# Kernel tuning notes

Hardware: AMD Instinct MI355X
Metric: run time of the kernel (lower is better)

Reference implementation:

```python
import jax, jax.numpy as jnp
import numpy as np

N, E, G, H = 4096, 8192, 64, 128  # nodes, edges, graphs, hidden dim
NODE_DIM, EDGE_DIM = 11, 5


def _linear_params(key, fan_in, fan_out):
    kw, kb = jax.random.split(key)
    s = 1.0 / np.sqrt(fan_in)
    w = jax.random.uniform(kw, (fan_in, fan_out), minval=-s, maxval=s, dtype=jnp.float32)
    b = jax.random.uniform(kb, (fan_out,), minval=-s, maxval=s, dtype=jnp.float32)
    return w, b


def setup_inputs() -> dict:
    key = jax.random.key(0)
    ks = jax.random.split(key, 10)
    x = jax.random.normal(ks[0], (N, NODE_DIM), dtype=jnp.float32)
    edge_attr = jax.random.normal(ks[1], (E, EDGE_DIM), dtype=jnp.float32)
    edge_index = jax.random.randint(ks[2], (2, E), 0, N, dtype=jnp.int64)
    batch = jnp.sort(jax.random.randint(ks[3], (N,), 0, G, dtype=jnp.int64))
    # preprocess MLP: node_dim -> 128 -> 128
    p1_w, p1_b = _linear_params(ks[4], NODE_DIM, H)
    p2_w, p2_b = _linear_params(ks[5], H, H)
    # edge net: edge_dim -> 128 -> 256 -> 128 -> 128*128 (ReLU between, none after last)
    e1_w, e1_b = _linear_params(ks[6], EDGE_DIM, 128)
    e2_w, e2_b = _linear_params(ks[7], 128, 256)
    e3_w, e3_b = _linear_params(ks[8], 256, 128)
    e4_w, e4_b = _linear_params(ks[9], 128, H * H)
    return {"x": x, "edge_attr": edge_attr, "edge_index": edge_index, "batch": batch,
            "p1_w": p1_w, "p1_b": p1_b, "p2_w": p2_w, "p2_b": p2_b,
            "e1_w": e1_w, "e1_b": e1_b, "e2_w": e2_w, "e2_b": e2_b,
            "e3_w": e3_w, "e3_b": e3_b, "e4_w": e4_w, "e4_b": e4_b}


def reference(x, edge_attr, edge_index, batch,
              p1_w, p1_b, p2_w, p2_b,
              e1_w, e1_b, e2_w, e2_b, e3_w, e3_b, e4_w, e4_b):
    # node preprocess MLP (maps 11-dim features to 128 so NNConv dims are consistent)
    h = jax.nn.relu(x @ p1_w + p1_b) @ p2_w + p2_b  # [N, H]
    # edge network -> per-edge weight matrix [E, H, H]
    e = jax.nn.relu(edge_attr @ e1_w + e1_b)
    e = jax.nn.relu(e @ e2_w + e2_b)
    e = jax.nn.relu(e @ e3_w + e3_b)
    W = (e @ e4_w + e4_b).reshape(E, H, H)
    # NNConv (root_weight=False, bias=False, aggr='mean'):
    src, dst = edge_index[0], edge_index[1]
    msg = jnp.einsum('ei,eio->eo', h[src], W)  # gather + per-edge matmul, [E, H]
    agg = jax.ops.segment_sum(msg, dst, num_segments=N)
    cnt = jax.ops.segment_sum(jnp.ones((E,), msg.dtype), dst, num_segments=N)
    h_out = agg / jnp.maximum(cnt, 1.0)[:, None]  # scatter-mean, [N, H]
    # global add pool over graphs
    pooled = jax.ops.segment_sum(h_out, batch, num_segments=G)  # [G, H]
    return pooled
```

## Files before the change

### kernel.cpp

```cpp
#include <hip/hip_runtime.h>
#include <hip/hip_bf16.h>

#define N_NODES 4096
#define N_EDGES 8192
#define N_GRAPHS 64
#define HDIM 128

typedef __attribute__((ext_vector_type(8))) short bf16x8;
typedef __attribute__((ext_vector_type(4))) float f32x4;
typedef __attribute__((ext_vector_type(4))) unsigned short u16x4;

static __device__ __forceinline__ unsigned short f2bf(float f) {
    unsigned u = __builtin_bit_cast(unsigned, f);
    u += 0x7fffu + ((u >> 16) & 1u);
    return (unsigned short)(u >> 16);
}
static __device__ __forceinline__ float bf2f(unsigned short s) {
    unsigned u = ((unsigned)s) << 16;
    return __builtin_bit_cast(float, u);
}

__global__ __launch_bounds__(256) void pre_kernel(
    const float* __restrict__ x, const float* __restrict__ p1w, const float* __restrict__ p1b,
    const float* __restrict__ p2w, const float* __restrict__ p2b, const float* __restrict__ e4b,
    unsigned short* __restrict__ h_bf, float* __restrict__ hb,
    const float* __restrict__ ea, const float* __restrict__ w1, const float* __restrict__ b1,
    const float* __restrict__ w4, unsigned short* __restrict__ w4perm,
    const float* __restrict__ w2, unsigned short* __restrict__ w2p,
    const float* __restrict__ w3, unsigned short* __restrict__ w3p,
    unsigned short* __restrict__ l1bf)
{
    __shared__ __align__(16) char smem[33024];
    const int t = threadIdx.x;
    const int bid = blockIdx.x;

    if (bid < 256) {
        float (*xs)[11]  = (float(*)[11])smem;
        float (*l1t)[16] = (float(*)[16])(smem + 704);
        float (*hs)[16]  = (float(*)[16])(smem + 8896);
        const int nb = bid;

        for (int r = t; r < 16 * 11; r += 256) {
            int e = r / 11, d = r % 11;
            xs[e][d] = x[(nb * 16 + e) * 11 + d];
        }
        __syncthreads();
        {
            int j = t & 127;
            float wd[11];
            #pragma unroll
            for (int d = 0; d < 11; ++d) wd[d] = p1w[d * 128 + j];
            float bj = p1b[j];
            for (int p = 0; p < 8; ++p) {
                int e = p * 2 + (t >> 7);
                float acc = bj;
                #pragma unroll
                for (int d = 0; d < 11; ++d) acc += xs[e][d] * wd[d];
                l1t[j][e] = fmaxf(acc, 0.f);
            }
        }
        __syncthreads();
        {
            int j = t & 127, eh = t >> 7;
            float acc[8];
            float bj = p2b[j];
            #pragma unroll
            for (int r = 0; r < 8; ++r) acc[r] = bj;
            for (int k = 0; k < 128; ++k) {
                float w = p2w[k * 128 + j];
                const float4* row = (const float4*)&l1t[k][eh * 8];
                float4 v0 = row[0], v1 = row[1];
                acc[0] += v0.x * w; acc[1] += v0.y * w; acc[2] += v0.z * w; acc[3] += v0.w * w;
                acc[4] += v1.x * w; acc[5] += v1.y * w; acc[6] += v1.z * w; acc[7] += v1.w * w;
            }
            #pragma unroll
            for (int r = 0; r < 8; ++r) {
                int e = eh * 8 + r;
                h_bf[(nb * 16 + e) * 128 + j] = f2bf(acc[r]);
                hs[j][e] = acc[r];
            }
        }
        __syncthreads();
        {
            int j = t & 127, eh = t >> 7;
            float acc[8] = {0.f,0.f,0.f,0.f,0.f,0.f,0.f,0.f};
            for (int i = 0; i < 128; ++i) {
                float w = e4b[i * 128 + j];
                const float4* row = (const float4*)&hs[i][eh * 8];
                float4 v0 = row[0], v1 = row[1];
                acc[0] += v0.x * w; acc[1] += v0.y * w; acc[2] += v0.z * w; acc[3] += v0.w * w;
                acc[4] += v1.x * w; acc[5] += v1.y * w; acc[6] += v1.z * w; acc[7] += v1.w * w;
            }
            #pragma unroll
            for (int r = 0; r < 8; ++r) hb[(nb * 16 + eh * 8 + r) * 128 + j] = acc[r];
        }
    } else if (bid < 384) {
        unsigned short (*tt)[129] = (unsigned short(*)[129])smem;
        const int i = bid - 256;
        for (int r = t; r < 16384; r += 256) {
            int k = r >> 7, o = r & 127;
            tt[o][k] = f2bf(w4[k * 16384 + i * 128 + o]);
        }
        __syncthreads();
        for (int r = t; r < 16384; r += 256) {
            int o = r >> 7, k = r & 127;
            w4perm[((size_t)(o >> 5) * 128 + i) * 4352 + (size_t)(o & 31) * 136 + k] = tt[o][k];
        }
    } else if (bid < 386) {
        unsigned short (*tt)[129] = (unsigned short(*)[129])smem;
        const int oh = bid - 384;
        for (int r = t; r < 16384; r += 256) {
            int k = r >> 7, ol = r & 127;
            tt[ol][k] = f2bf(w2[k * 256 + oh * 128 + ol]);
        }
        __syncthreads();
        for (int r = t; r < 16384; r += 256) {
            int ol = r >> 7, k = r & 127;
            w2p[(oh * 128 + ol) * 136 + k] = tt[ol][k];
        }
    } else if (bid < 388) {
        unsigned short (*tt)[257] = (unsigned short(*)[257])smem;
        const int oh = bid - 386;
        for (int r = t; r < 16384; r += 256) {
            int k = r >> 6, ol = r & 63;
            tt[ol][k] = f2bf(w3[k * 128 + oh * 64 + ol]);
        }
        __syncthreads();
        for (int r = t; r < 16384; r += 256) {
            int ol = r >> 8, k = r & 255;
            w3p[(oh * 64 + ol) * 264 + k] = tt[ol][k];
        }
    } else {
        float (*es)[5] = (float(*)[5])smem;
        const int eb = (bid - 388) * 128;
        for (int r = t; r < 640; r += 256) ((float*)es)[r] = ea[eb * 5 + r];
        __syncthreads();
        int j = t & 127, eh = t >> 7;
        float wd[5];
        #pragma unroll
        for (int d = 0; d < 5; ++d) wd[d] = w1[d * 128 + j];
        float bj = b1[j];
        for (int p = 0; p < 64; ++p) {
            int e = eh * 64 + p;
            float acc = bj;
            #pragma unroll
            for (int d = 0; d < 5; ++d) acc += es[e][d] * wd[d];
            l1bf[(size_t)(eb + e) * 128 + j] = f2bf(fmaxf(acc, 0.f));
        }
    }
}

__global__ __launch_bounds__(256, 2) void edge23_kernel(
    const unsigned short* __restrict__ l1bf,
    const float* __restrict__ b2, const float* __restrict__ b3,
    const unsigned short* __restrict__ w2p, const unsigned short* __restrict__ w3p,
    unsigned short* __restrict__ e3bf)
{
    __shared__ __align__(16) unsigned short l2a[32 * 264];
    const int t = threadIdx.x, bid = blockIdx.x;
    const int w = t >> 6, lane = t & 63, q = lane >> 4, l15 = lane & 15;
    const int e0 = bid * 32;
    const f32x4 zero4 = (f32x4){0.f, 0.f, 0.f, 0.f};

    bf16x8 afrag[2][4];
    #pragma unroll
    for (int mb = 0; mb < 2; ++mb)
        #pragma unroll
        for (int s = 0; s < 4; ++s)
            afrag[mb][s] = *(const bf16x8*)(l1bf + (size_t)(e0 + mb * 16 + l15) * 128 + s * 32 + q * 8);

    f32x4 acc[2][4];
    #pragma unroll
    for (int mb = 0; mb < 2; ++mb)
        #pragma unroll
        for (int ob = 0; ob < 4; ++ob) acc[mb][ob] = zero4;
    #pragma unroll
    for (int ob = 0; ob < 4; ++ob) {
        const int o = w * 64 + ob * 16 + l15;
        bf16x8 bfrag[4];
        #pragma unroll
        for (int s = 0; s < 4; ++s)
            bfrag[s] = *(const bf16x8*)(w2p + (size_t)o * 136 + s * 32 + q * 8);
        #pragma unroll
        for (int mb = 0; mb < 2; ++mb) {
            f32x4 tmp = __builtin_amdgcn_mfma_f32_16x16x32_bf16(afrag[mb][0], bfrag[0], zero4, 0, 0, 0);
            tmp = __builtin_amdgcn_mfma_f32_16x16x32_bf16(afrag[mb][1], bfrag[1], tmp, 0, 0, 0);
            tmp = __builtin_amdgcn_mfma_f32_16x16x32_bf16(afrag[mb][2], bfrag[2], tmp, 0, 0, 0);
            acc[mb][ob] = __builtin_amdgcn_mfma_f32_16x16x32_bf16(afrag[mb][3], bfrag[3], tmp, 0, 0, 0);
        }
    }
    #pragma unroll
    for (int mb = 0; mb < 2; ++mb)
        #pragma unroll
        for (int ob = 0; ob < 4; ++ob) {
            int o = w * 64 + ob * 16 + l15;
            float bo = b2[o];
            #pragma unroll
            for (int r = 0; r < 4; ++r) {
                int e_loc = mb * 16 + q * 4 + r;
                l2a[e_loc * 264 + o] = f2bf(fmaxf(acc[mb][ob][r] + bo, 0.f));
            }
        }
    __syncthreads();

    f32x4 acc3[2][2];
    #pragma unroll
    for (int mb = 0; mb < 2; ++mb)
        #pragma unroll
        for (int ob = 0; ob < 2; ++ob) acc3[mb][ob] = zero4;
    #pragma unroll
    for (int ks = 0; ks < 8; ++ks) {
        bf16x8 a3[2];
        #pragma unroll
        for (int mb = 0; mb < 2; ++mb)
            a3[mb] = *(const bf16x8*)&l2a[(mb * 16 + l15) * 264 + ks * 32 + q * 8];
        #pragma unroll
        for (int ob = 0; ob < 2; ++ob) {
            const int o = w * 32 + ob * 16 + l15;
            bf16x8 bf = *(const bf16x8*)(w3p + (size_t)o * 264 + ks * 32 + q * 8);
            #pragma unroll
            for (int mb = 0; mb < 2; ++mb)
                acc3[mb][ob] = __builtin_amdgcn_mfma_f32_16x16x32_bf16(a3[mb], bf, acc3[mb][ob], 0, 0, 0);
        }
    }
    #pragma unroll
    for (int mb = 0; mb < 2; ++mb)
        #pragma unroll
        for (int ob = 0; ob < 2; ++ob) {
            int o = w * 32 + ob * 16 + l15;
            float bo = b3[o];
            #pragma unroll
            for (int r = 0; r < 4; ++r) {
                int e = e0 + mb * 16 + q * 4 + r;
                e3bf[(size_t)e * 128 + o] = f2bf(fmaxf(acc3[mb][ob][r] + bo, 0.f));
            }
        }
}

__global__ __launch_bounds__(256, 2) void nnconv_kernel(
    const unsigned short* __restrict__ e3bf, const unsigned short* __restrict__ h_bf,
    const unsigned short* __restrict__ w4perm, const float* __restrict__ hb,
    const int* __restrict__ ei, float* __restrict__ agg, float* __restrict__ cnt)
{
    __shared__ __align__(16) unsigned short ht[128 * 128];
    __shared__ __align__(16) float red[3 * 128 * 16];
    const int t = threadIdx.x;
    const int bid = blockIdx.x;
    const int osplit = bid & 7;
    const int etile  = bid >> 3;
    const int w = t >> 6, lane = t & 63, q = lane >> 4, l15 = lane & 15;
    const int kpar = w;
    const int e0 = etile * 128;
    const int o0 = osplit * 16;

    bf16x8 afrag[8][4];
    #pragma unroll
    for (int mb = 0; mb < 8; ++mb)
        #pragma unroll
        for (int s = 0; s < 4; ++s) {
            int row = e0 + mb * 16 + l15;
            afrag[mb][s] = *(const bf16x8*)(e3bf + (size_t)row * 128 + s * 32 + q * 8);
        }
    #pragma unroll
    for (int mb = 0; mb < 8; ++mb)
        #pragma unroll
        for (int s = 0; s < 4; ++s)
            asm volatile("" : "+v"(afrag[mb][s]));
    asm volatile("" ::: "memory");

    {
        int r = t >> 1, part = t & 1;
        int s = ei[e0 + r];
        #pragma unroll
        for (int u = 0; u < 8; ++u) {
            uint4 v = *(const uint4*)(h_bf + (size_t)s * 128 + part * 64 + u * 8);
            const unsigned short* pv = (const unsigned short*)&v;
            #pragma unroll
            for (int j = 0; j < 8; ++j)
                ht[(part * 64 + u * 8 + j) * 128 + r] = pv[j];
        }
    }

    f32x4 acc[8];
    #pragma unroll
    for (int mb = 0; mb < 8; ++mb) acc[mb] = (f32x4){0.f, 0.f, 0.f, 0.f};
    const f32x4 zero4 = (f32x4){0.f, 0.f, 0.f, 0.f};

    __syncthreads();

    const unsigned short* bbase =
        w4perm + ((size_t)(osplit >> 1) * 128 + kpar * 32) * 4352
               + (size_t)((osplit & 1) * 16 + l15) * 136 + q * 8;
    bf16x8 bcur[4], bnxt[4];
    #pragma unroll
    for (int s = 0; s < 4; ++s) bcur[s] = *(const bf16x8*)(bbase + s * 32);
    for (int c = 0; c < 32; ++c) {
        if (c + 1 < 32) {
            const unsigned short* bp = bbase + (size_t)(c + 1) * 4352;
            #pragma unroll
            for (int s = 0; s < 4; ++s) bnxt[s] = *(const bf16x8*)(bp + s * 32);
        }
        const int gi = kpar * 32 + c;
        #pragma unroll
        for (int mb = 0; mb < 8; ++mb) {
            u16x4 hr = *(const u16x4*)&ht[gi * 128 + mb * 16 + q * 4];
            f32x4 tmp = __builtin_amdgcn_mfma_f32_16x16x32_bf16(afrag[mb][0], bcur[0], zero4, 0, 0, 0);
            tmp = __builtin_amdgcn_mfma_f32_16x16x32_bf16(afrag[mb][1], bcur[1], tmp, 0, 0, 0);
            tmp = __builtin_amdgcn_mfma_f32_16x16x32_bf16(afrag[mb][2], bcur[2], tmp, 0, 0, 0);
            tmp = __builtin_amdgcn_mfma_f32_16x16x32_bf16(afrag[mb][3], bcur[3], tmp, 0, 0, 0);
            #pragma unroll
            for (int r = 0; r < 4; ++r)
                acc[mb][r] += bf2f(hr[r]) * tmp[r];
        }
        #pragma unroll
        for (int s = 0; s < 4; ++s) bcur[s] = bnxt[s];
    }

    if (w > 0) {
        #pragma unroll
        for (int mb = 0; mb < 8; ++mb)
            #pragma unroll
            for (int r = 0; r < 4; ++r)
                red[((w - 1) * 128 + mb * 16 + q * 4 + r) * 16 + l15] = acc[mb][r];
    }
    __syncthreads();
    if (w == 0) {
        #pragma unroll
        for (int mb = 0; mb < 8; ++mb) {
            #pragma unroll
            for (int r = 0; r < 4; ++r) {
                int e_loc = mb * 16 + q * 4 + r;
                int e = e0 + e_loc;
                int de = ei[N_EDGES + e];
                int se = ei[e];
                int o = o0 + l15;
                float v = acc[mb][r]
                        + red[(0 * 128 + e_loc) * 16 + l15]
                        + red[(1 * 128 + e_loc) * 16 + l15]
                        + red[(2 * 128 + e_loc) * 16 + l15]
                        + hb[(size_t)se * 128 + o];
                if (osplit == 0 && l15 == 0) atomicAdd(&cnt[de], 1.0f);
                atomicAdd(&agg[(size_t)de * 128 + o], v);
            }
        }
    }
}

__global__ __launch_bounds__(128) void pool_kernel(
    const float* __restrict__ agg, const float* __restrict__ cnt,
    const int* __restrict__ batch, float* __restrict__ out)
{
    const int g = blockIdx.x, t = threadIdx.x;
    int lo = 0, hi = N_NODES;
    while (lo < hi) { int m = (lo + hi) >> 1; if (batch[m] < g) lo = m + 1; else hi = m; }
    const int n_lo = lo;
    int lo2 = n_lo, hi2 = N_NODES;
    while (lo2 < hi2) { int m = (lo2 + hi2) >> 1; if (batch[m] < g + 1) lo2 = m + 1; else hi2 = m; }
    const int n_hi = lo2;

    float s0 = 0.f, s1 = 0.f, s2 = 0.f, s3 = 0.f;
    int n = n_lo;
    for (; n + 4 <= n_hi; n += 4) {
        float c0 = cnt[n], c1 = cnt[n + 1], c2 = cnt[n + 2], c3 = cnt[n + 3];
        float v0 = agg[(n    ) * 128 + t];
        float v1 = agg[(n + 1) * 128 + t];
        float v2 = agg[(n + 2) * 128 + t];
        float v3 = agg[(n + 3) * 128 + t];
        s0 += v0 / (c0 > 1.f ? c0 : 1.f);
        s1 += v1 / (c1 > 1.f ? c1 : 1.f);
        s2 += v2 / (c2 > 1.f ? c2 : 1.f);
        s3 += v3 / (c3 > 1.f ? c3 : 1.f);
    }
    for (; n < n_hi; ++n) {
        float c = cnt[n];
        s0 += agg[n * 128 + t] / (c > 1.f ? c : 1.f);
    }
    out[g * 128 + t] = (s0 + s1) + (s2 + s3);
}

extern "C" void kernel_launch(void* const* d_in, const int* in_sizes, int n_in,
                              void* d_out, int out_size, void* d_ws, size_t ws_size,
                              hipStream_t stream)
{
    const float* x     = (const float*)d_in[0];
    const float* ea    = (const float*)d_in[1];
    const int*   ei    = (const int*)d_in[2];
    const int*   batch = (const int*)d_in[3];
    const float* p1w   = (const float*)d_in[4];
    const float* p1b   = (const float*)d_in[5];
    const float* p2w   = (const float*)d_in[6];
    const float* p2b   = (const float*)d_in[7];
    const float* w1    = (const float*)d_in[8];
    const float* b1    = (const float*)d_in[9];
    const float* w2    = (const float*)d_in[10];
    const float* b2    = (const float*)d_in[11];
    const float* w3    = (const float*)d_in[12];
    const float* b3    = (const float*)d_in[13];
    const float* w4    = (const float*)d_in[14];
    const float* b4    = (const float*)d_in[15];
    float* out = (float*)d_out;
    (void)in_sizes; (void)n_in; (void)out_size; (void)ws_size;

    char* ws = (char*)d_ws;
    unsigned short* h_bf = (unsigned short*)(ws);
    unsigned short* e3bf = (unsigned short*)(ws + 1048576);
    float* hb            = (float*)(ws + 3145728);
    unsigned short* w4p  = (unsigned short*)(ws + 5242880);
    float* agg           = (float*)(ws + 9699328);
    unsigned short* l1bf = (unsigned short*)(ws + 9699328);
    float* cnt           = (float*)(ws + 11796480);
    unsigned short* w2p  = (unsigned short*)(ws + 11812864);
    unsigned short* w3p  = (unsigned short*)(ws + 11882496);

    pre_kernel<<<452, 256, 0, stream>>>(
        x, p1w, p1b, p2w, p2b, b4, h_bf, hb,
        ea, w1, b1, w4, w4p, w2, w2p, w3, w3p, l1bf);
    edge23_kernel<<<256, 256, 0, stream>>>(l1bf, b2, b3, w2p, w3p, e3bf);
    hipMemsetAsync(agg, 0, (size_t)N_NODES * 128 * 4 + (size_t)N_NODES * 4, stream);
    nnconv_kernel<<<512, 256, 0, stream>>>(e3bf, h_bf, w4p, hb, ei, agg, cnt);
    pool_kernel<<<N_GRAPHS, 128, 0, stream>>>(agg, cnt, batch, out);
}
```

Baseline: 182.9 us.

## Deepen B-fragment prefetch, distribute epilogue reduction, and halve edge23 tile

The nnconv main loop now double-buffers two chunks of W4 fragments at a time and raises wave priority around the MFMA blocks. This is meant to hide global-load latency better. The cross-wave reduction now has all four waves write to padded shared memory and each handle a slice of edges for the atomics, instead of wave 0 doing all of it. edge23 processes 16 edges per block across twice as many blocks, and several scalar loops in pre_kernel get unroll pragmas. The changes add register pressure from the extra buffers and more shared memory for the reduction.

Result: slower. 220.1 us (+20.3%).

```diff
diff --git a/kernel.cpp b/kernel.cpp
--- a/kernel.cpp
+++ b/kernel.cpp
@@ -66,6 +66,7 @@
             float bj = p2b[j];
             #pragma unroll
             for (int r = 0; r < 8; ++r) acc[r] = bj;
+            #pragma unroll 8
             for (int k = 0; k < 128; ++k) {
                 float w = p2w[k * 128 + j];
                 const float4* row = (const float4*)&l1t[k][eh * 8];
@@ -84,6 +85,7 @@
         {
             int j = t & 127, eh = t >> 7;
             float acc[8] = {0.f,0.f,0.f,0.f,0.f,0.f,0.f,0.f};
+            #pragma unroll 8
             for (int i = 0; i < 128; ++i) {
                 float w = e4b[i * 128 + j];
                 const float4* row = (const float4*)&hs[i][eh * 8];
@@ -140,6 +142,7 @@
         #pragma unroll
         for (int d = 0; d < 5; ++d) wd[d] = w1[d * 128 + j];
         float bj = b1[j];
+        #pragma unroll 4
         for (int p = 0; p < 64; ++p) {
             int e = eh * 64 + p;
             float acc = bj;
@@ -156,24 +159,20 @@
     const unsigned short* __restrict__ w2p, const unsigned short* __restrict__ w3p,
     unsigned short* __restrict__ e3bf)
 {
-    __shared__ __align__(16) unsigned short l2a[32 * 264];
+    __shared__ __align__(16) unsigned short l2a[16 * 264];
     const int t = threadIdx.x, bid = blockIdx.x;
     const int w = t >> 6, lane = t & 63, q = lane >> 4, l15 = lane & 15;
-    const int e0 = bid * 32;
+    const int e0 = bid * 16;
     const f32x4 zero4 = (f32x4){0.f, 0.f, 0.f, 0.f};
 
-    bf16x8 afrag[2][4];
-    #pragma unroll
-    for (int mb = 0; mb < 2; ++mb)
-        #pragma unroll
-        for (int s = 0; s < 4; ++s)
-            afrag[mb][s] = *(const bf16x8*)(l1bf + (size_t)(e0 + mb * 16 + l15) * 128 + s * 32 + q * 8);
-
-    f32x4 acc[2][4];
-    #pragma unroll
-    for (int mb = 0; mb < 2; ++mb)
-        #pragma unroll
-        for (int ob = 0; ob < 4; ++ob) acc[mb][ob] = zero4;
+    bf16x8 afrag[4];
+    #pragma unroll
+    for (int s = 0; s < 4; ++s)
+        afrag[s] = *(const bf16x8*)(l1bf + (size_t)(e0 + l15) * 128 + s * 32 + q * 8);
+
+    f32x4 acc[4];
+    #pragma unroll
+    for (int ob = 0; ob < 4; ++ob) acc[ob] = zero4;
     #pragma unroll
     for (int ob = 0; ob < 4; ++ob) {
         const int o = w * 64 + ob * 16 + l15;
@@ -181,60 +180,45 @@
         #pragma unroll
         for (int s = 0; s < 4; ++s)
             bfrag[s] = *(const bf16x8*)(w2p + (size_t)o * 136 + s * 32 + q * 8);
-        #pragma unroll
-        for (int mb = 0; mb < 2; ++mb) {
-            f32x4 tmp = __builtin_amdgcn_mfma_f32_16x16x32_bf16(afrag[mb][0], bfrag[0], zero4, 0, 0, 0);
-            tmp = __builtin_amdgcn_mfma_f32_16x16x32_bf16(afrag[mb][1], bfrag[1], tmp, 0, 0, 0);
-            tmp = __builtin_amdgcn_mfma_f32_16x16x32_bf16(afrag[mb][2], bfrag[2], tmp, 0, 0, 0);
-            acc[mb][ob] = __builtin_amdgcn_mfma_f32_16x16x32_bf16(afrag[mb][3], bfrag[3], tmp, 0, 0, 0);
-        }
-    }
-    #pragma unroll
-    for (int mb = 0; mb < 2; ++mb)
-        #pragma unroll
-        for (int ob = 0; ob < 4; ++ob) {
-            int o = w * 64 + ob * 16 + l15;
-            float bo = b2[o];
-            #pragma unroll
-            for (int r = 0; r < 4; ++r) {
-                int e_loc = mb * 16 + q * 4 + r;
-                l2a[e_loc * 264 + o] = f2bf(fmaxf(acc[mb][ob][r] + bo, 0.f));
-            }
-        }
+        f32x4 tmp = __builtin_amdgcn_mfma_f32_16x16x32_bf16(afrag[0], bfrag[0], zero4, 0, 0, 0);
+        tmp = __builtin_amdgcn_mfma_f32_16x16x32_bf16(afrag[1], bfrag[1], tmp, 0, 0, 0);
+        tmp = __builtin_amdgcn_mfma_f32_16x16x32_bf16(afrag[2], bfrag[2], tmp, 0, 0, 0);
+        acc[ob] = __builtin_amdgcn_mfma_f32_16x16x32_bf16(afrag[3], bfrag[3], tmp, 0, 0, 0);
+    }
+    #pragma unroll
+    for (int ob = 0; ob < 4; ++ob) {
+        int o = w * 64 + ob * 16 + l15;
+        float bo = b2[o];
+        #pragma unroll
+        for (int r = 0; r < 4; ++r) {
+            int e_loc = q * 4 + r;
+            l2a[e_loc * 264 + o] = f2bf(fmaxf(acc[ob][r] + bo, 0.f));
+        }
+    }
     __syncthreads();
 
-    f32x4 acc3[2][2];
-    #pragma unroll
-    for (int mb = 0; mb < 2; ++mb)
-        #pragma unroll
-        for (int ob = 0; ob < 2; ++ob) acc3[mb][ob] = zero4;
+    f32x4 acc3[2];
+    acc3[0] = zero4; acc3[1] = zero4;
     #pragma unroll
     for (int ks = 0; ks < 8; ++ks) {
-        bf16x8 a3[2];
-        #pragma unroll
-        for (int mb = 0; mb < 2; ++mb)
-            a3[mb] = *(const bf16x8*)&l2a[(mb * 16 + l15) * 264 + ks * 32 + q * 8];
+        bf16x8 a3 = *(const bf16x8*)&l2a[l15 * 264 + ks * 32 + q * 8];
         #pragma unroll
         for (int ob = 0; ob < 2; ++ob) {
             const int o = w * 32 + ob * 16 + l15;
             bf16x8 bf = *(const bf16x8*)(w3p + (size_t)o * 264 + ks * 32 + q * 8);
-            #pragma unroll
-            for (int mb = 0; mb < 2; ++mb)
-                acc3[mb][ob] = __builtin_amdgcn_mfma_f32_16x16x32_bf16(a3[mb], bf, acc3[mb][ob], 0, 0, 0);
-        }
-    }
-    #pragma unroll
-    for (int mb = 0; mb < 2; ++mb)
-        #pragma unroll
-        for (int ob = 0; ob < 2; ++ob) {
-            int o = w * 32 + ob * 16 + l15;
-            float bo = b3[o];
-            #pragma unroll
-            for (int r = 0; r < 4; ++r) {
-                int e = e0 + mb * 16 + q * 4 + r;
-                e3bf[(size_t)e * 128 + o] = f2bf(fmaxf(acc3[mb][ob][r] + bo, 0.f));
-            }
-        }
+            acc3[ob] = __builtin_amdgcn_mfma_f32_16x16x32_bf16(a3, bf, acc3[ob], 0, 0, 0);
+        }
+    }
+    #pragma unroll
+    for (int ob = 0; ob < 2; ++ob) {
+        int o = w * 32 + ob * 16 + l15;
+        float bo = b3[o];
+        #pragma unroll
+        for (int r = 0; r < 4; ++r) {
+            int e = e0 + q * 4 + r;
+            e3bf[(size_t)e * 128 + o] = f2bf(fmaxf(acc3[ob][r] + bo, 0.f));
+        }
+    }
 }
 
 __global__ __launch_bounds__(256, 2) void nnconv_kernel(
@@ -243,7 +227,7 @@
     const int* __restrict__ ei, float* __restrict__ agg, float* __restrict__ cnt)
 {
     __shared__ __align__(16) unsigned short ht[128 * 128];
-    __shared__ __align__(16) float red[3 * 128 * 16];
+    __shared__ __align__(16) float red[4 * 128 * 17];
     const int t = threadIdx.x;
     const int bid = blockIdx.x;
     const int osplit = bid & 7;
@@ -261,12 +245,6 @@
             int row = e0 + mb * 16 + l15;
             afrag[mb][s] = *(const bf16x8*)(e3bf + (size_t)row * 128 + s * 32 + q * 8);
         }
-    #pragma unroll
-    for (int mb = 0; mb < 8; ++mb)
-        #pragma unroll
-        for (int s = 0; s < 4; ++s)
-            asm volatile("" : "+v"(afrag[mb][s]));
-    asm volatile("" ::: "memory");
 
     {
         int r = t >> 1, part = t & 1;
@@ -291,58 +269,59 @@
     const unsigned short* bbase =
         w4perm + ((size_t)(osplit >> 1) * 128 + kpar * 32) * 4352
                + (size_t)((osplit & 1) * 16 + l15) * 136 + q * 8;
-    bf16x8 bcur[4], bnxt[4];
-    #pragma unroll
-    for (int s = 0; s < 4; ++s) bcur[s] = *(const bf16x8*)(bbase + s * 32);
-    for (int c = 0; c < 32; ++c) {
-        if (c + 1 < 32) {
-            const unsigned short* bp = bbase + (size_t)(c + 1) * 4352;
-            #pragma unroll
-            for (int s = 0; s < 4; ++s) bnxt[s] = *(const bf16x8*)(bp + s * 32);
-        }
-        const int gi = kpar * 32 + c;
+
+    auto LB = [&](int c, bf16x8* dst) {
+        const unsigned short* bp = bbase + (size_t)c * 4352;
+        #pragma unroll
+        for (int s = 0; s < 4; ++s) dst[s] = *(const bf16x8*)(bp + s * 32);
+    };
+    auto COMPUTE = [&](const bf16x8* b, int gi) {
         #pragma unroll
         for (int mb = 0; mb < 8; ++mb) {
             u16x4 hr = *(const u16x4*)&ht[gi * 128 + mb * 16 + q * 4];
-            f32x4 tmp = __builtin_amdgcn_mfma_f32_16x16x32_bf16(afrag[mb][0], bcur[0], zero4, 0, 0, 0);
-            tmp = __builtin_amdgcn_mfma_f32_16x16x32_bf16(afrag[mb][1], bcur[1], tmp, 0, 0, 0);
-            tmp = __builtin_amdgcn_mfma_f32_16x16x32_bf16(afrag[mb][2], bcur[2], tmp, 0, 0, 0);
-            tmp = __builtin_amdgcn_mfma_f32_16x16x32_bf16(afrag[mb][3], bcur[3], tmp, 0, 0, 0);
+            f32x4 tmp = __builtin_amdgcn_mfma_f32_16x16x32_bf16(afrag[mb][0], b[0], zero4, 0, 0, 0);
+            tmp = __builtin_amdgcn_mfma_f32_16x16x32_bf16(afrag[mb][1], b[1], tmp, 0, 0, 0);
+            tmp = __builtin_amdgcn_mfma_f32_16x16x32_bf16(afrag[mb][2], b[2], tmp, 0, 0, 0);
+            tmp = __builtin_amdgcn_mfma_f32_16x16x32_bf16(afrag[mb][3], b[3], tmp, 0, 0, 0);
             #pragma unroll
             for (int r = 0; r < 4; ++r)
                 acc[mb][r] += bf2f(hr[r]) * tmp[r];
         }
-        #pragma unroll
-        for (int s = 0; s < 4; ++s) bcur[s] = bnxt[s];
-    }
-
-    if (w > 0) {
-        #pragma unroll
-        for (int mb = 0; mb < 8; ++mb)
-            #pragma unroll
-            for (int r = 0; r < 4; ++r)
-                red[((w - 1) * 128 + mb * 16 + q * 4 + r) * 16 + l15] = acc[mb][r];
-    }
+    };
+
+    bf16x8 bA[4], bB[4], bC[4], bD[4];
+    LB(0, bA); LB(1, bB);
+    for (int cc = 0; cc < 32; cc += 2) {
+        if (cc + 2 < 32) LB(cc + 2, bC);
+        if (cc + 3 < 32) LB(cc + 3, bD);
+        __builtin_amdgcn_s_setprio(1);
+        COMPUTE(bA, kpar * 32 + cc);
+        COMPUTE(bB, kpar * 32 + cc + 1);
+        __builtin_amdgcn_s_setprio(0);
+        #pragma unroll
+        for (int s = 0; s < 4; ++s) { bA[s] = bC[s]; bB[s] = bD[s]; }
+    }
+
+    #pragma unroll
+    for (int mb = 0; mb < 8; ++mb)
+        #pragma unroll
+        for (int r = 0; r < 4; ++r)
+            red[(w * 128 + mb * 16 + q * 4 + r) * 17 + l15] = acc[mb][r];
     __syncthreads();
-    if (w == 0) {
-        #pragma unroll
-        for (int mb = 0; mb < 8; ++mb) {
-            #pragma unroll
-            for (int r = 0; r < 4; ++r) {
-                int e_loc = mb * 16 + q * 4 + r;
-                int e = e0 + e_loc;
-                int de = ei[N_EDGES + e];
-                int se = ei[e];
-                int o = o0 + l15;
-                float v = acc[mb][r]
-                        + red[(0 * 128 + e_loc) * 16 + l15]
-                        + red[(1 * 128 + e_loc) * 16 + l15]
-                        + red[(2 * 128 + e_loc) * 16 + l15]
-                        + hb[(size_t)se * 128 + o];
-                if (osplit == 0 && l15 == 0) atomicAdd(&cnt[de], 1.0f);
-                atomicAdd(&agg[(size_t)de * 128 + o], v);
-            }
-        }
+    #pragma unroll
+    for (int er = 0; er < 8; ++er) {
+        int e_loc = w * 32 + q * 8 + er;
+        int e = e0 + e_loc;
+        int de = ei[N_EDGES + e];
+        int se = ei[e];
+        int o = o0 + l15;
+        float v = red[(0 * 128 + e_loc) * 17 + l15]
+                + red[(1 * 128 + e_loc) * 17 + l15]
+                + red[(2 * 128 + e_loc) * 17 + l15]
+                + red[(3 * 128 + e_loc) * 17 + l15]
+                + hb[(size_t)se * 128 + o];
+        if (osplit == 0 && l15 == 0) atomicAdd(&cnt[de], 1.0f);
+        atomicAdd(&agg[(size_t)de * 128 + o], v);
     }
 }
 
@@ -415,7 +394,7 @@
     pre_kernel<<<452, 256, 0, stream>>>(
         x, p1w, p1b, p2w, p2b, b4, h_bf, hb,
         ea, w1, b1, w4, w4p, w2, w2p, w3, w3p, l1bf);
-    edge23_kernel<<<256, 256, 0, stream>>>(l1bf, b2, b3, w2p, w3p, e3bf);
+    edge23_kernel<<<512, 256, 0, stream>>>(l1bf, b2, b3, w2p, w3p, e3bf);
     hipMemsetAsync(agg, 0, (size_t)N_NODES * 128 * 4 + (size_t)N_NODES * 4, stream);
     nnconv_kernel<<<512, 256, 0, stream>>>(e3bf, h_bf, w4p, hb, ei, agg, cnt);
     pool_kernel<<<N_GRAPHS, 128, 0, stream>>>(agg, cnt, batch, out);
```
